# Performance work log

Measured on AMD Instinct MI355X. Metric: run time of the kernel, lower is better.

## Reference

```python
import jax, jax.numpy as jnp
import numpy as np

DK = 64

def setup_inputs() -> dict:
    key = jax.random.key(0)
    kq, kk, kv = jax.random.split(key, 3)
    B, S, dk, dv = 16, 2048, 64, 64
    q = jax.random.normal(kq, (B, S, dk), dtype=jnp.float32)
    k = jax.random.normal(kk, (B, S, dk), dtype=jnp.float32)
    v = jax.random.normal(kv, (B, S, dv), dtype=jnp.float32)
    return {"q": q, "k": k, "v": v}

def reference(q, k, v):
    # scores: [B, Sq, Sk], scaled by 1/sqrt(dk)
    scale = 1.0 / jnp.sqrt(jnp.asarray(DK, dtype=q.dtype))
    scores = jnp.einsum('bqd,bkd->bqk', q, k) * scale
    attn = jax.nn.softmax(scores, axis=-1)
    return jnp.einsum('bqk,bkd->bqd', attn, v)
```

## Files before the change

### kernel.cpp

```cpp
#include <hip/hip_runtime.h>
#include <hip/hip_fp16.h>

#define SLEN 2048

typedef _Float16 half8_t  __attribute__((ext_vector_type(8)));
typedef __fp16   fp16x2_t __attribute__((ext_vector_type(2)));
typedef float    floatx16 __attribute__((ext_vector_type(16)));
typedef float    float2v  __attribute__((ext_vector_type(2)));

#define MFMA(a, b, c) __builtin_amdgcn_mfma_f32_32x32x16_f16((a), (b), (c), 0, 0, 0)

typedef const __attribute__((address_space(1))) void gvoid_t;
typedef __attribute__((address_space(3))) void lvoid_t;

__device__ __forceinline__ void gload_lds16(const void* g, void* l) {
    __builtin_amdgcn_global_load_lds((gvoid_t*)g, (lvoid_t*)l, 16, 0, 0);
}

__device__ __forceinline__ int bswap23(int r) {
    return (r & ~12) | ((r & 4) << 1) | ((r & 8) >> 1);
}

#define QSCALE 0.18033688011112042f
#define CINIT  -5.770780163555854f

__device__ __forceinline__ floatx16 zero16() {
    floatx16 z;
    #pragma unroll
    for (int i = 0; i < 16; ++i) z[i] = 0.0f;
    return z;
}

__device__ __forceinline__ floatx16 initC() {
    floatx16 z;
    #pragma unroll
    for (int i = 0; i < 16; ++i) z[i] = CINIT;
    return z;
}

union PU { fp16x2_t h2[4]; half8_t h8; };

__global__ __launch_bounds__(256)
void prep_kernel(const float* __restrict__ Kg, const float* __restrict__ Vg,
                 _Float16* __restrict__ KP, _Float16* __restrict__ VP)
{
    __shared__ _Float16 kt[32][72];
    __shared__ _Float16 vt[32][72];
    const int t = threadIdx.x;
    const int T = blockIdx.x;
    const size_t row0 = (size_t)T * 32;

    {
        const int r = t >> 3, c0 = (t & 7) * 8;
        const float* kp = Kg + (row0 + r) * 64 + c0;
        const float* vp = Vg + (row0 + r) * 64 + c0;
        float4 a0 = *(const float4*)kp;
        float4 a1 = *(const float4*)(kp + 4);
        float4 b0 = *(const float4*)vp;
        float4 b1 = *(const float4*)(vp + 4);
        kt[r][c0 + 0] = (_Float16)a0.x; kt[r][c0 + 1] = (_Float16)a0.y;
        kt[r][c0 + 2] = (_Float16)a0.z; kt[r][c0 + 3] = (_Float16)a0.w;
        kt[r][c0 + 4] = (_Float16)a1.x; kt[r][c0 + 5] = (_Float16)a1.y;
        kt[r][c0 + 6] = (_Float16)a1.z; kt[r][c0 + 7] = (_Float16)a1.w;
        vt[r][c0 + 0] = (_Float16)b0.x; vt[r][c0 + 1] = (_Float16)b0.y;
        vt[r][c0 + 2] = (_Float16)b0.z; vt[r][c0 + 3] = (_Float16)b0.w;
        vt[r][c0 + 4] = (_Float16)b1.x; vt[r][c0 + 5] = (_Float16)b1.y;
        vt[r][c0 + 6] = (_Float16)b1.z; vt[r][c0 + 7] = (_Float16)b1.w;
    }
    __syncthreads();

    const int hi  = (t >> 5) & 1;
    const int col = t & 31;

    {
        const int dc = t >> 6;
        half8_t ko;
        #pragma unroll
        for (int j = 0; j < 8; ++j) ko[j] = kt[col][dc * 16 + hi * 8 + j];
        *(half8_t*)(KP + (size_t)T * 2048 + t * 8) = ko;
    }
    {
        const int g = t >> 6, kc = g & 1, nc = g >> 1;
        half8_t vo;
        #pragma unroll
        for (int j = 0; j < 8; ++j)
            vo[j] = vt[bswap23(kc * 16 + hi * 8 + j)][nc * 32 + col];
        *(half8_t*)(VP + (size_t)T * 2048 + t * 8) = vo;
    }
}

__global__ __launch_bounds__(256, 2)
void fattn_kernel(const float* __restrict__ Qg, const _Float16* __restrict__ KP,
                  const _Float16* __restrict__ VP, float* __restrict__ Og)
{
    __shared__ __align__(16) _Float16 ring[4 * 2 * 4096];
    __shared__ float lbufl[4][2][32];
    __shared__ float lbuf2[2][32];

    const int tid  = threadIdx.x;
    const int w    = tid >> 6;
    const int lane = tid & 63;
    const int h    = lane >> 5;
    const int col  = lane & 31;

    const int p  = blockIdx.x;
    const int b  = ((p >> 8) << 3) | (p & 7);
    const int qb = (p >> 3) & 31;

    half8_t qhi[2][4], qlo[2][4];
    #pragma unroll
    for (int s = 0; s < 2; ++s) {
        const size_t qrow = (size_t)b * SLEN + (size_t)qb * 64 + s * 32 + col;
        const float* qp = Qg + qrow * 64 + h * 8;
        #pragma unroll
        for (int dc = 0; dc < 4; ++dc) {
            float4 f0 = *(const float4*)(qp + dc * 16);
            float4 f1 = *(const float4*)(qp + dc * 16 + 4);
            float v[8] = {f0.x, f0.y, f0.z, f0.w, f1.x, f1.y, f1.z, f1.w};
            #pragma unroll
            for (int j = 0; j < 8; ++j) {
                float x = v[j] * QSCALE;
                _Float16 hi16 = (_Float16)x;
                qhi[s][dc][j] = hi16;
                qlo[s][dc][j] = (_Float16)(x - (float)hi16);
            }
        }
    }

    _Float16* myring = ring + w * 8192;
    const char* KPb = (const char*)KP;
    const char* VPb = (const char*)VP;

    auto stage = [&](int buf, int t) {
        const size_t off = ((size_t)(b * 64 + w * 16 + t)) << 12;
        const char* ks = KPb + off + lane * 16;
        const char* vs = VPb + off + lane * 16;
        _Float16* d = myring + buf * 4096;
        gload_lds16(ks,        d);
        gload_lds16(ks + 1024, d + 512);
        gload_lds16(ks + 2048, d + 1024);
        gload_lds16(ks + 3072, d + 1536);
        gload_lds16(vs,        d + 2048);
        gload_lds16(vs + 1024, d + 2560);
        gload_lds16(vs + 2048, d + 3072);
        gload_lds16(vs + 3072, d + 3584);
    };

    floatx16 o00 = zero16(), o01 = zero16(), o10 = zero16(), o11 = zero16();
    float2v la0A = {0.0f, 0.0f}, la0B = {0.0f, 0.0f};
    float2v la1A = {0.0f, 0.0f}, la1B = {0.0f, 0.0f};

    stage(0, 0);

#define EXPPK(SS, U, J, ACC) {                                        \
    float e0 = __builtin_amdgcn_exp2f(SS[2*(J)]);                     \
    float e1 = __builtin_amdgcn_exp2f(SS[2*(J)+1]);                   \
    float2v e2 = {e0, e1};                                            \
    ACC += e2;                                                        \
    (U).h2[(J) & 3] = __builtin_amdgcn_cvt_pkrtz(e0, e1); }

    for (int t = 0; t < 16; ++t) {
        const int cur = t & 1;
        if (t < 15) {
            stage(1 - cur, t + 1);
            asm volatile("s_waitcnt vmcnt(8)" ::: "memory");
        } else {
            asm volatile("s_waitcnt vmcnt(0)" ::: "memory");
        }

        _Float16* kb = myring + cur * 4096;
        _Float16* vb = kb + 2048;

        half8_t kf[4];
        #pragma unroll
        for (int dc = 0; dc < 4; ++dc)
            kf[dc] = *(half8_t*)(kb + dc * 512 + lane * 8);

        floatx16 sa0 = zero16(), sb0 = initC();
        floatx16 sa1 = zero16(), sb1 = initC();

        sa0 = MFMA(kf[0], qhi[0][0], sa0);
        sb0 = MFMA(kf[2], qhi[0][2], sb0);
        sa0 = MFMA(kf[0], qlo[0][0], sa0);
        sb0 = MFMA(kf[2], qlo[0][2], sb0);
        sa0 = MFMA(kf[1], qhi[0][1], sa0);
        sb0 = MFMA(kf[3], qhi[0][3], sb0);
        sa0 = MFMA(kf[1], qlo[0][1], sa0);
        sb0 = MFMA(kf[3], qlo[0][3], sb0);

        half8_t vf[4];
        #pragma unroll
        for (int g = 0; g < 4; ++g)
            vf[g] = *(half8_t*)(vb + g * 512 + lane * 8);

        floatx16 ss0 = sa0 + sb0;
        PU u0, u1;
        sa1 = MFMA(kf[0], qhi[1][0], sa1); EXPPK(ss0, u0, 0, la0A)
        sb1 = MFMA(kf[2], qhi[1][2], sb1); EXPPK(ss0, u0, 1, la0B)
        sa1 = MFMA(kf[0], qlo[1][0], sa1); EXPPK(ss0, u0, 2, la0A)
        sb1 = MFMA(kf[2], qlo[1][2], sb1); EXPPK(ss0, u0, 3, la0B)
        sa1 = MFMA(kf[1], qhi[1][1], sa1); EXPPK(ss0, u1, 4, la0A)
        sb1 = MFMA(kf[3], qhi[1][3], sb1); EXPPK(ss0, u1, 5, la0B)
        sa1 = MFMA(kf[1], qlo[1][1], sa1); EXPPK(ss0, u1, 6, la0A)
        sb1 = MFMA(kf[3], qlo[1][3], sb1); EXPPK(ss0, u1, 7, la0B)

        half8_t pf00 = u0.h8, pf01 = u1.h8;

        floatx16 ss1 = sa1 + sb1;
        PU u2, u3;
        o00 = MFMA(pf00, vf[0], o00);
        EXPPK(ss1, u2, 0, la1A) EXPPK(ss1, u2, 1, la1B)
        o01 = MFMA(pf00, vf[2], o01);
        EXPPK(ss1, u2, 2, la1A) EXPPK(ss1, u2, 3, la1B)
        o00 = MFMA(pf01, vf[1], o00);
        EXPPK(ss1, u3, 4, la1A) EXPPK(ss1, u3, 5, la1B)
        o01 = MFMA(pf01, vf[3], o01);
        EXPPK(ss1, u3, 6, la1A) EXPPK(ss1, u3, 7, la1B)

        half8_t pf10 = u2.h8, pf11 = u3.h8;

        o10 = MFMA(pf10, vf[0], o10);
        o11 = MFMA(pf10, vf[2], o11);
        o10 = MFMA(pf11, vf[1], o10);
        o11 = MFMA(pf11, vf[3], o11);
    }
#undef EXPPK

    float la0 = la0A[0] + la0A[1] + la0B[0] + la0B[1];
    float la1 = la1A[0] + la1A[1] + la1B[0] + la1B[1];

    float lw0 = la0 + __shfl_xor(la0, 32, 64);
    float lw1 = la1 + __shfl_xor(la1, 32, 64);

    float* cb = (float*)ring;

#define ODUMP(d, g, acc) { _Pragma("unroll") \
    for (int r = 0; r < 16; ++r) (d)[(((g)*16 + r)*2 + h)*32 + col] = (acc)[r]; }
#define OADD(d, g, acc) { _Pragma("unroll") \
    for (int r = 0; r < 16; ++r) (acc)[r] += (d)[(((g)*16 + r)*2 + h)*32 + col]; }

    __syncthreads();
    if (w >= 2) {
        float* d = cb + (w - 2) * 4096;
        ODUMP(d, 0, o00) ODUMP(d, 1, o01) ODUMP(d, 2, o10) ODUMP(d, 3, o11)
        if (h == 0) { lbufl[w][0][col] = lw0; lbufl[w][1][col] = lw1; }
    }
    __syncthreads();
    if (w < 2) {
        float* d = cb + w * 4096;
        OADD(d, 0, o00) OADD(d, 1, o01) OADD(d, 2, o10) OADD(d, 3, o11)
        lw0 += lbufl[w + 2][0][col];
        lw1 += lbufl[w + 2][1][col];
    }
    __syncthreads();
    if (w == 1) {
        ODUMP(cb, 0, o00) ODUMP(cb, 1, o01) ODUMP(cb, 2, o10) ODUMP(cb, 3, o11)
        if (h == 0) { lbufl[1][0][col] = lw0; lbufl[1][1][col] = lw1; }
    }
    __syncthreads();
    if (w == 0) {
        OADD(cb, 0, o00) OADD(cb, 1, o01) OADD(cb, 2, o10) OADD(cb, 3, o11)
        lw0 += lbufl[1][0][col];
        lw1 += lbufl[1][1][col];
        if (h == 0) { lbuf2[0][col] = lw0; lbuf2[1][col] = lw1; }
    }
    __syncthreads();
    if (w == 0) {
        float* ob = cb + 8192;
        #pragma unroll
        for (int r = 0; r < 16; ++r) {
            const int qr = (r & 3) + 8 * (r >> 2) + 4 * h;
            const float li0 = 1.0f / lbuf2[0][qr];
            const float li1 = 1.0f / lbuf2[1][qr];
            ob[(0 * 32 + qr) * 64 +  0 + col] = o00[r] * li0;
            ob[(0 * 32 + qr) * 64 + 32 + col] = o01[r] * li0;
            ob[(1 * 32 + qr) * 64 +  0 + col] = o10[r] * li1;
            ob[(1 * 32 + qr) * 64 + 32 + col] = o11[r] * li1;
        }
    }
    __syncthreads();
    {
        const float* ob = cb + 8192;
        const int q = tid >> 2, ch = tid & 3;
        float4 x0 = *(const float4*)(ob + q * 64 + ch * 16);
        float4 x1 = *(const float4*)(ob + q * 64 + ch * 16 + 4);
        float4 x2 = *(const float4*)(ob + q * 64 + ch * 16 + 8);
        float4 x3 = *(const float4*)(ob + q * 64 + ch * 16 + 12);
        float* op = Og + ((size_t)b * SLEN + (size_t)qb * 64 + q) * 64 + ch * 16;
        *(float4*)(op)      = x0;
        *(float4*)(op + 4)  = x1;
        *(float4*)(op + 8)  = x2;
        *(float4*)(op + 12) = x3;
    }
#undef ODUMP
#undef OADD
}

extern "C" void kernel_launch(void* const* d_in, const int* in_sizes, int n_in,
                              void* d_out, int out_size, void* d_ws, size_t ws_size,
                              hipStream_t stream) {
    const float* q = (const float*)d_in[0];
    const float* k = (const float*)d_in[1];
    const float* v = (const float*)d_in[2];
    float* o = (float*)d_out;

    _Float16* KP = (_Float16*)d_ws;
    _Float16* VP = KP + (size_t)1024 * 2048;
    (void)ws_size; (void)in_sizes; (void)n_in; (void)out_size;

    prep_kernel<<<dim3(1024), dim3(256), 0, stream>>>(k, v, KP, VP);
    fattn_kernel<<<dim3(512), dim3(256), 0, stream>>>(q, KP, VP, o);
}
```

Baseline: 107.2 us.

## Halve query tile per block, single-buffer K/V ring, double grid and occupancy

Each block now handles 32 query rows instead of 64, so the grid doubles to 1024 blocks and the launch-bounds occupancy hint rises from 2 to 4. The per-wave double-buffered LDS ring becomes single-buffered. The next tile's load is issued only after the QK MFMAs have read K/V into registers, with explicit waits and a sched barrier. This is meant to give more parallelism across the device and more waves per CU to hide latency. In exchange, K/V are reloaded twice as often per query and overlap within a wave is reduced.

```diff
diff --git a/kernel.cpp b/kernel.cpp
--- a/kernel.cpp
+++ b/kernel.cpp
@@ -89,13 +89,13 @@
     }
 }
 
-__global__ __launch_bounds__(256, 2)
+__global__ __launch_bounds__(256, 4)
 void fattn_kernel(const float* __restrict__ Qg, const _Float16* __restrict__ KP,
                   const _Float16* __restrict__ VP, float* __restrict__ Og)
 {
-    __shared__ __align__(16) _Float16 ring[4 * 2 * 4096];
-    __shared__ float lbufl[4][2][32];
-    __shared__ float lbuf2[2][32];
+    __shared__ __align__(16) _Float16 ring[4 * 4096];
+    __shared__ float lbufl[4][32];
+    __shared__ float lbuf2[32];
 
     const int tid  = threadIdx.x;
     const int w    = tid >> 6;
@@ -104,13 +104,12 @@
     const int col  = lane & 31;
 
     const int p  = blockIdx.x;
-    const int b  = ((p >> 8) << 3) | (p & 7);
-    const int qb = (p >> 3) & 31;
-
-    half8_t qhi[2][4], qlo[2][4];
-    #pragma unroll
-    for (int s = 0; s < 2; ++s) {
-        const size_t qrow = (size_t)b * SLEN + (size_t)qb * 64 + s * 32 + col;
+    const int b  = ((p >> 9) << 3) | (p & 7);
+    const int qb = (p >> 3) & 63;
+
+    half8_t qhi[4], qlo[4];
+    {
+        const size_t qrow = (size_t)b * SLEN + (size_t)qb * 32 + col;
         const float* qp = Qg + qrow * 64 + h * 8;
         #pragma unroll
         for (int dc = 0; dc < 4; ++dc) {
@@ -121,21 +120,21 @@
             for (int j = 0; j < 8; ++j) {
                 float x = v[j] * QSCALE;
                 _Float16 hi16 = (_Float16)x;
-                qhi[s][dc][j] = hi16;
-                qlo[s][dc][j] = (_Float16)(x - (float)hi16);
+                qhi[dc][j] = hi16;
+                qlo[dc][j] = (_Float16)(x - (float)hi16);
             }
         }
     }
 
-    _Float16* myring = ring + w * 8192;
+    _Float16* myring = ring + w * 4096;
     const char* KPb = (const char*)KP;
     const char* VPb = (const char*)VP;
 
-    auto stage = [&](int buf, int t) {
+    auto stage = [&](int t) {
         const size_t off = ((size_t)(b * 64 + w * 16 + t)) << 12;
         const char* ks = KPb + off + lane * 16;
         const char* vs = VPb + off + lane * 16;
-        _Float16* d = myring + buf * 4096;
+        _Float16* d = myring;
         gload_lds16(ks,        d);
         gload_lds16(ks + 1024, d + 512);
         gload_lds16(ks + 2048, d + 1024);
@@ -146,11 +145,10 @@
         gload_lds16(vs + 3072, d + 3584);
     };
 
-    floatx16 o00 = zero16(), o01 = zero16(), o10 = zero16(), o11 = zero16();
-    float2v la0A = {0.0f, 0.0f}, la0B = {0.0f, 0.0f};
-    float2v la1A = {0.0f, 0.0f}, la1B = {0.0f, 0.0f};
-
-    stage(0, 0);
+    floatx16 o0 = zero16(), o1 = zero16();
+    float2v laA = {0.0f, 0.0f}, laB = {0.0f, 0.0f};
+
+    stage(0);
 
 #define EXPPK(SS, U, J, ACC) {                                        \
     float e0 = __builtin_amdgcn_exp2f(SS[2*(J)]);                     \
@@ -160,77 +158,49 @@
     (U).h2[(J) & 3] = __builtin_amdgcn_cvt_pkrtz(e0, e1); }
 
     for (int t = 0; t < 16; ++t) {
-        const int cur = t & 1;
-        if (t < 15) {
-            stage(1 - cur, t + 1);
-            asm volatile("s_waitcnt vmcnt(8)" ::: "memory");
-        } else {
-            asm volatile("s_waitcnt vmcnt(0)" ::: "memory");
-        }
-
-        _Float16* kb = myring + cur * 4096;
-        _Float16* vb = kb + 2048;
-
-        half8_t kf[4];
+        asm volatile("s_waitcnt vmcnt(0)" ::: "memory");
+
+        half8_t kf[4], vf[4];
         #pragma unroll
         for (int dc = 0; dc < 4; ++dc)
-            kf[dc] = *(half8_t*)(kb + dc * 512 + lane * 8);
-
-        floatx16 sa0 = zero16(), sb0 = initC();
-        floatx16 sa1 = zero16(), sb1 = initC();
-
-        sa0 = MFMA(kf[0], qhi[0][0], sa0);
-        sb0 = MFMA(kf[2], qhi[0][2], sb0);
-        sa0 = MFMA(kf[0], qlo[0][0], sa0);
-        sb0 = MFMA(kf[2], qlo[0][2], sb0);
-        sa0 = MFMA(kf[1], qhi[0][1], sa0);
-        sb0 = MFMA(kf[3], qhi[0][3], sb0);
-        sa0 = MFMA(kf[1], qlo[0][1], sa0);
-        sb0 = MFMA(kf[3], qlo[0][3], sb0);
-
-        half8_t vf[4];
+            kf[dc] = *(half8_t*)(myring + dc * 512 + lane * 8);
         #pragma unroll
         for (int g = 0; g < 4; ++g)
-            vf[g] = *(half8_t*)(vb + g * 512 + lane * 8);
-
-        floatx16 ss0 = sa0 + sb0;
+            vf[g] = *(half8_t*)(myring + 2048 + g * 512 + lane * 8);
+
+        floatx16 sa = zero16(), sb = initC();
+
+        sa = MFMA(kf[0], qhi[0], sa);
+        sb = MFMA(kf[2], qhi[2], sb);
+        sa = MFMA(kf[0], qlo[0], sa);
+        sb = MFMA(kf[2], qlo[2], sb);
+        sa = MFMA(kf[1], qhi[1], sa);
+        sb = MFMA(kf[3], qhi[3], sb);
+        sa = MFMA(kf[1], qlo[1], sa);
+        sb = MFMA(kf[3], qlo[3], sb);
+
+        asm volatile("s_waitcnt lgkmcnt(0)" ::: "memory");
+        __builtin_amdgcn_sched_barrier(0);
+        if (t < 15) stage(t + 1);
+
+        floatx16 ss = sa + sb;
         PU u0, u1;
-        sa1 = MFMA(kf[0], qhi[1][0], sa1); EXPPK(ss0, u0, 0, la0A)
-        sb1 = MFMA(kf[2], qhi[1][2], sb1); EXPPK(ss0, u0, 1, la0B)
-        sa1 = MFMA(kf[0], qlo[1][0], sa1); EXPPK(ss0, u0, 2, la0A)
-        sb1 = MFMA(kf[2], qlo[1][2], sb1); EXPPK(ss0, u0, 3, la0B)
-        sa1 = MFMA(kf[1], qhi[1][1], sa1); EXPPK(ss0, u1, 4, la0A)
-        sb1 = MFMA(kf[3], qhi[1][3], sb1); EXPPK(ss0, u1, 5, la0B)
-        sa1 = MFMA(kf[1], qlo[1][1], sa1); EXPPK(ss0, u1, 6, la0A)
-        sb1 = MFMA(kf[3], qlo[1][3], sb1); EXPPK(ss0, u1, 7, la0B)
-
-        half8_t pf00 = u0.h8, pf01 = u1.h8;
-
-        floatx16 ss1 = sa1 + sb1;
-        PU u2, u3;
-        o00 = MFMA(pf00, vf[0], o00);
-        EXPPK(ss1, u2, 0, la1A) EXPPK(ss1, u2, 1, la1B)
-        o01 = MFMA(pf00, vf[2], o01);
-        EXPPK(ss1, u2, 2, la1A) EXPPK(ss1, u2, 3, la1B)
-        o00 = MFMA(pf01, vf[1], o00);
-        EXPPK(ss1, u3, 4, la1A) EXPPK(ss1, u3, 5, la1B)
-        o01 = MFMA(pf01, vf[3], o01);
-        EXPPK(ss1, u3, 6, la1A) EXPPK(ss1, u3, 7, la1B)
-
-        half8_t pf10 = u2.h8, pf11 = u3.h8;
-
-        o10 = MFMA(pf10, vf[0], o10);
-        o11 = MFMA(pf10, vf[2], o11);
-        o10 = MFMA(pf11, vf[1], o10);
-        o11 = MFMA(pf11, vf[3], o11);
+        EXPPK(ss, u0, 0, laA) EXPPK(ss, u0, 1, laB)
+        EXPPK(ss, u0, 2, laA) EXPPK(ss, u0, 3, laB)
+        EXPPK(ss, u1, 4, laA) EXPPK(ss, u1, 5, laB)
+        EXPPK(ss, u1, 6, laA) EXPPK(ss, u1, 7, laB)
+        half8_t pf0 = u0.h8, pf1 = u1.h8;
+
+        o0 = MFMA(pf0, vf[0], o0);
+        o1 = MFMA(pf0, vf[2], o1);
+        o0 = MFMA(pf1, vf[1], o0);
+        o1 = MFMA(pf1, vf[3], o1);
     }
 #undef EXPPK
 
-    float la0 = la0A[0] + la0A[1] + la0B[0] + la0B[1];
-    float la1 = la1A[0] + la1A[1] + la1B[0] + la1B[1];
-
-    float lw0 = la0 + __shfl_xor(la0, 32, 64);
-    float lw1 = la1 + __shfl_xor(la1, 32, 64);
+    float la = laA[0] + laA[1] + laB[0] + laB[1];
+
+    float lw = la + __shfl_xor(la, 32, 64);
 
     float* cb = (float*)ring;
 
@@ -241,56 +211,47 @@
 
     __syncthreads();
     if (w >= 2) {
-        float* d = cb + (w - 2) * 4096;
-        ODUMP(d, 0, o00) ODUMP(d, 1, o01) ODUMP(d, 2, o10) ODUMP(d, 3, o11)
-        if (h == 0) { lbufl[w][0][col] = lw0; lbufl[w][1][col] = lw1; }
+        float* d = cb + (w - 2) * 2048;
+        ODUMP(d, 0, o0) ODUMP(d, 1, o1)
+        if (h == 0) lbufl[w][col] = lw;
     }
     __syncthreads();
     if (w < 2) {
-        float* d = cb + w * 4096;
-        OADD(d, 0, o00) OADD(d, 1, o01) OADD(d, 2, o10) OADD(d, 3, o11)
-        lw0 += lbufl[w + 2][0][col];
-        lw1 += lbufl[w + 2][1][col];
+        float* d = cb + w * 2048;
+        OADD(d, 0, o0) OADD(d, 1, o1)
+        lw += lbufl[w + 2][col];
     }
     __syncthreads();
     if (w == 1) {
-        ODUMP(cb, 0, o00) ODUMP(cb, 1, o01) ODUMP(cb, 2, o10) ODUMP(cb, 3, o11)
-        if (h == 0) { lbufl[1][0][col] = lw0; lbufl[1][1][col] = lw1; }
+        ODUMP(cb, 0, o0) ODUMP(cb, 1, o1)
+        if (h == 0) lbufl[1][col] = lw;
     }
     __syncthreads();
     if (w == 0) {
-        OADD(cb, 0, o00) OADD(cb, 1, o01) OADD(cb, 2, o10) OADD(cb, 3, o11)
-        lw0 += lbufl[1][0][col];
-        lw1 += lbufl[1][1][col];
-        if (h == 0) { lbuf2[0][col] = lw0; lbuf2[1][col] = lw1; }
+        OADD(cb, 0, o0) OADD(cb, 1, o1)
+        lw += lbufl[1][col];
+        if (h == 0) lbuf2[col] = lw;
     }
     __syncthreads();
     if (w == 0) {
-        float* ob = cb + 8192;
+        float* ob = cb + 4096;
         #pragma unroll
         for (int r = 0; r < 16; ++r) {
             const int qr = (r & 3) + 8 * (r >> 2) + 4 * h;
-            const float li0 = 1.0f / lbuf2[0][qr];
-            const float li1 = 1.0f / lbuf2[1][qr];
-            ob[(0 * 32 + qr) * 64 +  0 + col] = o00[r] * li0;
-            ob[(0 * 32 + qr) * 64 + 32 + col] = o01[r] * li0;
-            ob[(1 * 32 + qr) * 64 +  0 + col] = o10[r] * li1;
-            ob[(1 * 32 + qr) * 64 + 32 + col] = o11[r] * li1;
+            const float li = 1.0f / lbuf2[qr];
+            ob[qr * 64 +  0 + col] = o0[r] * li;
+            ob[qr * 64 + 32 + col] = o1[r] * li;
         }
     }
     __syncthreads();
     {
-        const float* ob = cb + 8192;
-        const int q = tid >> 2, ch = tid & 3;
-        float4 x0 = *(const float4*)(ob + q * 64 + ch * 16);
-        float4 x1 = *(const float4*)(ob + q * 64 + ch * 16 + 4);
-        float4 x2 = *(const float4*)(ob + q * 64 + ch * 16 + 8);
-        float4 x3 = *(const float4*)(ob + q * 64 + ch * 16 + 12);
-        float* op = Og + ((size_t)b * SLEN + (size_t)qb * 64 + q) * 64 + ch * 16;
-        *(float4*)(op)      = x0;
-        *(float4*)(op + 4)  = x1;
-        *(float4*)(op + 8)  = x2;
-        *(float4*)(op + 12) = x3;
+        const float* ob = cb + 4096;
+        const int row = tid >> 3, ch = tid & 7;
+        float4 x0 = *(const float4*)(ob + row * 64 + ch * 8);
+        float4 x1 = *(const float4*)(ob + row * 64 + ch * 8 + 4);
+        float* op = Og + ((size_t)b * SLEN + (size_t)qb * 32 + row) * 64 + ch * 8;
+        *(float4*)(op)     = x0;
+        *(float4*)(op + 4) = x1;
     }
 #undef ODUMP
 #undef OADD
@@ -309,5 +270,5 @@
     (void)ws_size; (void)in_sizes; (void)n_in; (void)out_size;
 
     prep_kernel<<<dim3(1024), dim3(256), 0, stream>>>(k, v, KP, VP);
-    fattn_kernel<<<dim3(512), dim3(256), 0, stream>>>(q, KP, VP, o);
-}
+    fattn_kernel<<<dim3(1024), dim3(256), 0, stream>>>(q, KP, VP, o);
+}
```

Result: slower. 116.8 us (+8.9%).

## Load K/V tiles directly into registers with two-deep prefetch instead of LDS

Applied to the files above, without the earlier changes.

Replaces the async global-to-LDS staging ring, with its explicit vmcnt waits and LDS reads, by direct global loads of the pre-packed K and V fragments into registers. Two tiles are held in flight in alternating register sets, and the next-but-one tile is refilled in the middle of the current body. This removes LDS traffic and the LDS round trip per tile. In exchange it raises VGPR pressure (32 extra half8 registers) under a launch bound of 2 blocks, and relies on the compiler placing waitcnts well. The shared buffer is shrunk to only what the output reduction needs.

```diff
diff --git a/kernel.cpp b/kernel.cpp
--- a/kernel.cpp
+++ b/kernel.cpp
@@ -9,13 +9,6 @@
 typedef float    float2v  __attribute__((ext_vector_type(2)));
 
 #define MFMA(a, b, c) __builtin_amdgcn_mfma_f32_32x32x16_f16((a), (b), (c), 0, 0, 0)
-
-typedef const __attribute__((address_space(1))) void gvoid_t;
-typedef __attribute__((address_space(3))) void lvoid_t;
-
-__device__ __forceinline__ void gload_lds16(const void* g, void* l) {
-    __builtin_amdgcn_global_load_lds((gvoid_t*)g, (lvoid_t*)l, 16, 0, 0);
-}
 
 __device__ __forceinline__ int bswap23(int r) {
     return (r & ~12) | ((r & 4) << 1) | ((r & 8) >> 1);
@@ -93,7 +86,7 @@
 void fattn_kernel(const float* __restrict__ Qg, const _Float16* __restrict__ KP,
                   const _Float16* __restrict__ VP, float* __restrict__ Og)
 {
-    __shared__ __align__(16) _Float16 ring[4 * 2 * 4096];
+    __shared__ __align__(16) float cbuf[12288];
     __shared__ float lbufl[4][2][32];
     __shared__ float lbuf2[2][32];
 
@@ -127,30 +120,27 @@
         }
     }
 
-    _Float16* myring = ring + w * 8192;
     const char* KPb = (const char*)KP;
     const char* VPb = (const char*)VP;
 
-    auto stage = [&](int buf, int t) {
+    auto loadT = [&](int t, half8_t* kr, half8_t* vr) {
         const size_t off = ((size_t)(b * 64 + w * 16 + t)) << 12;
-        const char* ks = KPb + off + lane * 16;
-        const char* vs = VPb + off + lane * 16;
-        _Float16* d = myring + buf * 4096;
-        gload_lds16(ks,        d);
-        gload_lds16(ks + 1024, d + 512);
-        gload_lds16(ks + 2048, d + 1024);
-        gload_lds16(ks + 3072, d + 1536);
-        gload_lds16(vs,        d + 2048);
-        gload_lds16(vs + 1024, d + 2560);
-        gload_lds16(vs + 2048, d + 3072);
-        gload_lds16(vs + 3072, d + 3584);
+        const _Float16* ks = (const _Float16*)(KPb + off) + lane * 8;
+        const _Float16* vs = (const _Float16*)(VPb + off) + lane * 8;
+        #pragma unroll
+        for (int c = 0; c < 4; ++c) {
+            kr[c] = *(const half8_t*)(ks + c * 512);
+            vr[c] = *(const half8_t*)(vs + c * 512);
+        }
     };
 
     floatx16 o00 = zero16(), o01 = zero16(), o10 = zero16(), o11 = zero16();
     float2v la0A = {0.0f, 0.0f}, la0B = {0.0f, 0.0f};
     float2v la1A = {0.0f, 0.0f}, la1B = {0.0f, 0.0f};
 
-    stage(0, 0);
+    half8_t kA[4], vA[4], kB[4], vB[4];
+    loadT(0, kA, vA);
+    loadT(1, kB, vB);
 
 #define EXPPK(SS, U, J, ACC) {                                        \
     float e0 = __builtin_amdgcn_exp2f(SS[2*(J)]);                     \
@@ -159,71 +149,69 @@
     ACC += e2;                                                        \
     (U).h2[(J) & 3] = __builtin_amdgcn_cvt_pkrtz(e0, e1); }
 
-    for (int t = 0; t < 16; ++t) {
-        const int cur = t & 1;
-        if (t < 15) {
-            stage(1 - cur, t + 1);
-            asm volatile("s_waitcnt vmcnt(8)" ::: "memory");
-        } else {
-            asm volatile("s_waitcnt vmcnt(0)" ::: "memory");
-        }
-
-        _Float16* kb = myring + cur * 4096;
-        _Float16* vb = kb + 2048;
-
-        half8_t kf[4];
-        #pragma unroll
-        for (int dc = 0; dc < 4; ++dc)
-            kf[dc] = *(half8_t*)(kb + dc * 512 + lane * 8);
-
-        floatx16 sa0 = zero16(), sb0 = initC();
-        floatx16 sa1 = zero16(), sb1 = initC();
-
-        sa0 = MFMA(kf[0], qhi[0][0], sa0);
-        sb0 = MFMA(kf[2], qhi[0][2], sb0);
-        sa0 = MFMA(kf[0], qlo[0][0], sa0);
-        sb0 = MFMA(kf[2], qlo[0][2], sb0);
-        sa0 = MFMA(kf[1], qhi[0][1], sa0);
-        sb0 = MFMA(kf[3], qhi[0][3], sb0);
-        sa0 = MFMA(kf[1], qlo[0][1], sa0);
-        sb0 = MFMA(kf[3], qlo[0][3], sb0);
-
-        half8_t vf[4];
-        #pragma unroll
-        for (int g = 0; g < 4; ++g)
-            vf[g] = *(half8_t*)(vb + g * 512 + lane * 8);
-
-        floatx16 ss0 = sa0 + sb0;
-        PU u0, u1;
-        sa1 = MFMA(kf[0], qhi[1][0], sa1); EXPPK(ss0, u0, 0, la0A)
-        sb1 = MFMA(kf[2], qhi[1][2], sb1); EXPPK(ss0, u0, 1, la0B)
-        sa1 = MFMA(kf[0], qlo[1][0], sa1); EXPPK(ss0, u0, 2, la0A)
-        sb1 = MFMA(kf[2], qlo[1][2], sb1); EXPPK(ss0, u0, 3, la0B)
-        sa1 = MFMA(kf[1], qhi[1][1], sa1); EXPPK(ss0, u1, 4, la0A)
-        sb1 = MFMA(kf[3], qhi[1][3], sb1); EXPPK(ss0, u1, 5, la0B)
-        sa1 = MFMA(kf[1], qlo[1][1], sa1); EXPPK(ss0, u1, 6, la0A)
-        sb1 = MFMA(kf[3], qlo[1][3], sb1); EXPPK(ss0, u1, 7, la0B)
-
-        half8_t pf00 = u0.h8, pf01 = u1.h8;
-
-        floatx16 ss1 = sa1 + sb1;
-        PU u2, u3;
-        o00 = MFMA(pf00, vf[0], o00);
-        EXPPK(ss1, u2, 0, la1A) EXPPK(ss1, u2, 1, la1B)
-        o01 = MFMA(pf00, vf[2], o01);
-        EXPPK(ss1, u2, 2, la1A) EXPPK(ss1, u2, 3, la1B)
-        o00 = MFMA(pf01, vf[1], o00);
-        EXPPK(ss1, u3, 4, la1A) EXPPK(ss1, u3, 5, la1B)
-        o01 = MFMA(pf01, vf[3], o01);
-        EXPPK(ss1, u3, 6, la1A) EXPPK(ss1, u3, 7, la1B)
-
-        half8_t pf10 = u2.h8, pf11 = u3.h8;
-
-        o10 = MFMA(pf10, vf[0], o10);
-        o11 = MFMA(pf10, vf[2], o11);
-        o10 = MFMA(pf11, vf[1], o10);
-        o11 = MFMA(pf11, vf[3], o11);
-    }
+#define BODY(T, KC, VC)                                                       \
+{                                                                             \
+    floatx16 sa0 = zero16(), sb0 = initC();                                   \
+    floatx16 sa1 = zero16(), sb1 = initC();                                   \
+                       \
+    sa0 = MFMA(KC[0], qhi[0][0], sa0);                                        \
+    sb0 = MFMA(KC[2], qhi[0][2], sb0);                                        \
+    sa0 = MFMA(KC[0], qlo[0][0], sa0);                                        \
+    sb0 = MFMA(KC[2], qlo[0][2], sb0);                                        \
+    sa0 = MFMA(KC[1], qhi[0][1], sa0);                                        \
+    sb0 = MFMA(KC[3], qhi[0][3], sb0);                                        \
+    sa0 = MFMA(KC[1], qlo[0][1], sa0);                                        \
+    sb0 = MFMA(KC[3], qlo[0][3], sb0);                                        \
+                         \
+    floatx16 ss0 = sa0 + sb0;                                                 \
+    PU u0, u1;                                                                \
+    sa1 = MFMA(KC[0], qhi[1][0], sa1); EXPPK(ss0, u0, 0, la0A)                \
+    sb1 = MFMA(KC[2], qhi[1][2], sb1); EXPPK(ss0, u0, 1, la0B)                \
+    sa1 = MFMA(KC[0], qlo[1][0], sa1); EXPPK(ss0, u0, 2, la0A)                \
+    sb1 = MFMA(KC[2], qlo[1][2], sb1); EXPPK(ss0, u0, 3, la0B)                \
+    sa1 = MFMA(KC[1], qhi[1][1], sa1); EXPPK(ss0, u1, 4, la0A)                \
+    sb1 = MFMA(KC[3], qhi[1][3], sb1); EXPPK(ss0, u1, 5, la0B)                \
+    sa1 = MFMA(KC[1], qlo[1][1], sa1); EXPPK(ss0, u1, 6, la0A)                \
+    sb1 = MFMA(KC[3], qlo[1][3], sb1); EXPPK(ss0, u1, 7, la0B)                \
+    half8_t pf00 = u0.h8, pf01 = u1.h8;                                       \
+                 \
+    if ((T) + 2 < 16) {                                                       \
+        const size_t off2 = ((size_t)(b * 64 + w * 16 + (T) + 2)) << 12;      \
+        const _Float16* ks2 = (const _Float16*)(KPb + off2) + lane * 8;       \
+        _Pragma("unroll")                                                     \
+        for (int c = 0; c < 4; ++c) KC[c] = *(const half8_t*)(ks2 + c * 512); \
+    }                                                                         \
+                         \
+    floatx16 ss1 = sa1 + sb1;                                                 \
+    PU u2, u3;                                                                \
+    o00 = MFMA(pf00, VC[0], o00);                                             \
+    EXPPK(ss1, u2, 0, la1A) EXPPK(ss1, u2, 1, la1B)                           \
+    o01 = MFMA(pf00, VC[2], o01);                                             \
+    EXPPK(ss1, u2, 2, la1A) EXPPK(ss1, u2, 3, la1B)                           \
+    o00 = MFMA(pf01, VC[1], o00);                                             \
+    EXPPK(ss1, u3, 4, la1A) EXPPK(ss1, u3, 5, la1B)                           \
+    o01 = MFMA(pf01, VC[3], o01);                                             \
+    EXPPK(ss1, u3, 6, la1A) EXPPK(ss1, u3, 7, la1B)                           \
+    half8_t pf10 = u2.h8, pf11 = u3.h8;                                       \
+                                                         \
+    o10 = MFMA(pf10, VC[0], o10);                                             \
+    o11 = MFMA(pf10, VC[2], o11);                                             \
+    o10 = MFMA(pf11, VC[1], o10);                                             \
+    o11 = MFMA(pf11, VC[3], o11);                                             \
+                                 \
+    if ((T) + 2 < 16) {                                                       \
+        const size_t off2 = ((size_t)(b * 64 + w * 16 + (T) + 2)) << 12;      \
+        const _Float16* vs2 = (const _Float16*)(VPb + off2) + lane * 8;       \
+        _Pragma("unroll")                                                     \
+        for (int c = 0; c < 4; ++c) VC[c] = *(const half8_t*)(vs2 + c * 512); \
+    }                                                                         \
+}
+
+    for (int tt = 0; tt < 16; tt += 2) {
+        BODY(tt,     kA, vA);
+        BODY(tt + 1, kB, vB);
+    }
+#undef BODY
 #undef EXPPK
 
     float la0 = la0A[0] + la0A[1] + la0B[0] + la0B[1];
@@ -232,7 +220,7 @@
     float lw0 = la0 + __shfl_xor(la0, 32, 64);
     float lw1 = la1 + __shfl_xor(la1, 32, 64);
 
-    float* cb = (float*)ring;
+    float* cb = cbuf;
 
 #define ODUMP(d, g, acc) { _Pragma("unroll") \
     for (int r = 0; r < 16; ++r) (d)[(((g)*16 + r)*2 + h)*32 + col] = (acc)[r]; }
```

Measured after the change: 168.7 us. 57.3% more time.
